# Performance work log

Hardware: AMD Instinct MI355X
Metric: run time of the kernel (lower is better)

## Reference

```python
import jax, jax.numpy as jnp
import numpy as np

B, S, D, VOCAB = 64, 2048, 256, 288

def setup_inputs() -> dict:
    key = jax.random.key(0)
    k1, k2, k3 = jax.random.split(key, 3)
    TE = jax.random.randint(k1, (B, S, 2), 0, VOCAB, dtype=jnp.int64)
    W1 = jax.random.normal(k2, (VOCAB + 7, D), dtype=jnp.float32) * 0.05
    b1 = jnp.zeros((D,), dtype=jnp.float32)
    W2 = jax.random.normal(k3, (D, D), dtype=jnp.float32) * 0.05
    b2 = jnp.zeros((D,), dtype=jnp.float32)
    return {"TE": TE, "T": VOCAB, "W1": W1, "b1": b1, "W2": W2, "b2": b2}

def reference(TE, T, W1, b1, W2, b2):
    # one_hot(day,7)||one_hot(time,T) @ W1  ==  gather rows of W1 and add
    day = TE[..., 0].astype(jnp.int32) % 7          # [B, S]
    tod = TE[..., 1].astype(jnp.int32) % T          # [B, S]
    h = W1[day] + W1[7 + tod] + b1                  # [B, S, D]  (Linear 1)
    h = jax.nn.relu(h)
    out = jnp.einsum('bsd,de->bse', h, W2) + b2     # [B, S, D]  (Linear 2)
    return out[:, :, None, :]                       # [B, S, 1, D]
```

## Files before the change

kernel.cpp:

```cpp
#include <hip/hip_runtime.h>
#include <hip/hip_bf16.h>


typedef __bf16 bf16x4 __attribute__((ext_vector_type(4)));
typedef __bf16 bf16x8 __attribute__((ext_vector_type(8)));
typedef float  f32x4  __attribute__((ext_vector_type(4)));

#define M_TOTAL   131072
#define BM        128
#define HPAD      258


__global__ __launch_bounds__(64) void prep_all(const float* __restrict__ W1,
                                               const float* __restrict__ b1,
                                               const float* __restrict__ W2,
                                               __bf16* __restrict__ W2S,
                                               __bf16* __restrict__ Htab,
                                               const int* __restrict__ TE32,
                                               int* __restrict__ flag, int T) {
    const int b = blockIdx.x, lane = threadIdx.x;
    const int nTab = 7 * T;
    if (b < nTab) {
        const float* __restrict__ wa = W1 + (b / T) * 256;
        const float* __restrict__ wb = W1 + (7 + b % T) * 256;
        f32x4 a = *(const f32x4*)(wa + lane * 4);
        f32x4 c = *(const f32x4*)(wb + lane * 4);
        f32x4 d = *(const f32x4*)(b1 + lane * 4);
        bf16x4 h;
#pragma unroll
        for (int j = 0; j < 4; ++j) h[j] = (__bf16)fmaxf(a[j] + c[j] + d[j], 0.0f);
        *(bf16x4*)(Htab + b * 256 + lane * 4) = h;
    } else {
        const int wb = b - nTab;
#pragma unroll
        for (int q = 0; q < 2; ++q) {
            int c = (wb * 64 + lane) * 2 + q;
            int l = c & 63, ksnt = c >> 6;
            int ks = ksnt & 7, nt = ksnt >> 3;
            int n  = nt * 16 + (l & 15);
            int k0 = ks * 32 + (l >> 4) * 8;
            bf16x8 w;
#pragma unroll
            for (int j = 0; j < 8; ++j) w[j] = (__bf16)W2[(k0 + j) * 256 + n];
            *(bf16x8*)(W2S + c * 8) = w;
        }
        if (wb == 0) {
            int v = 0;
            for (int i = lane; i < 2048; i += 64) v |= TE32[2 * i + 1];
            unsigned long long nz = __ballot(v != 0);
            if (lane == 0) *flag = (nz == 0ull) ? 1 : 0;
        }
    }
}

__global__ __launch_bounds__(256, 4) void temb_gemm(
        const int*   __restrict__ TE32,
        const __bf16* __restrict__ Htab,
        const __bf16* __restrict__ W2S,
        const float* __restrict__ b2,
        const int*   __restrict__ flag,
        float* __restrict__ out, int T)
{
    __shared__ __bf16 hbuf[4][16 * HPAD];
    const int is64 = *flag;
    const int wave = threadIdx.x >> 6;
    const int lane = threadIdx.x & 63;
    const int m    = lane & 15;
    const int quad = lane >> 4;
    const int half = lane >> 5;
    const int c32  = lane & 31;
    const int rowBase = blockIdx.x * BM + wave * 32;
    __bf16* __restrict__ myH = &hbuf[wave][0];

    int code = 0;
    if (lane < 32) {
        int day, tod;
        if (is64) { int4 te = *(const int4*)(TE32 + 4 * (rowBase + lane)); day = te.x; tod = te.z; }
        else      { int2 te = *(const int2*)(TE32 + 2 * (rowBase + lane)); day = te.x; tod = te.y; }
        code = (day % 7) * T + tod % T;
    }

    bf16x8 afrag[2][8];
#pragma unroll
    for (int t = 0; t < 2; ++t) {
#pragma unroll
        for (int g = 0; g < 8; ++g) {
            const int ridx = __shfl(code, t * 16 + 2 * g + half);
            bf16x8 hv = *(const bf16x8*)(Htab + ridx * 256 + c32 * 8);
            *(bf16x8*)(myH + (2 * g + half) * HPAD + c32 * 8) = hv;
        }
#pragma unroll
        for (int ks = 0; ks < 8; ++ks)
            afrag[t][ks] = *(const bf16x8*)(myH + m * HPAD + ks * 32 + quad * 8);
    }

    float b2r[16];
#pragma unroll
    for (int nt = 0; nt < 16; ++nt) b2r[nt] = b2[nt * 16 + m];

    const __bf16* __restrict__ wp = W2S + lane * 8;
#pragma unroll 4
    for (int nt = 0; nt < 16; ++nt) {
        f32x4 acc0 = {0.f, 0.f, 0.f, 0.f};
        f32x4 acc1 = {0.f, 0.f, 0.f, 0.f};
#pragma unroll
        for (int ks = 0; ks < 8; ++ks) {
            bf16x8 bfrag = *(const bf16x8*)(wp + (nt * 8 + ks) * 512);
            acc0 = __builtin_amdgcn_mfma_f32_16x16x32_bf16(afrag[0][ks], bfrag, acc0, 0, 0, 0);
            acc1 = __builtin_amdgcn_mfma_f32_16x16x32_bf16(afrag[1][ks], bfrag, acc1, 0, 0, 0);
        }
        const int ncol = nt * 16 + m;
        const float bias = b2r[nt];
#pragma unroll
        for (int r = 0; r < 4; ++r) {
            const int row0 = rowBase + quad * 4 + r;
            out[row0 * 256 + ncol]        = acc0[r] + bias;
            out[(row0 + 16) * 256 + ncol] = acc1[r] + bias;
        }
    }
}

extern "C" void kernel_launch(void* const* d_in, const int* in_sizes, int n_in,
                              void* d_out, int out_size, void* d_ws, size_t ws_size,
                              hipStream_t stream) {
    const int*   TE = (const int*)  d_in[0];
    const float* W1 = (const float*)d_in[2];
    const float* b1 = (const float*)d_in[3];
    const float* W2 = (const float*)d_in[4];
    const float* b2 = (const float*)d_in[5];
    const int T = in_sizes[2] / 256 - 7;

    __bf16* W2S  = (__bf16*)d_ws;
    __bf16* Htab = (__bf16*)((char*)d_ws + 131072);
    int*    flag = (int*)((char*)d_ws + 131072 + (size_t)7 * T * 256 * 2);
    float*  out  = (float*)d_out;

    prep_all<<<7 * T + 64, 64, 0, stream>>>(W1, b1, W2, W2S, Htab, TE, flag, T);
    temb_gemm<<<M_TOTAL / BM, 256, 0, stream>>>(TE, Htab, W2S, b2, flag, out, T);
}
```

Before: 178.2 us.

## Stage W2 through shared memory and swap MFMA operands for vectorized stores

The GEMM kernel no longer gathers H rows through LDS; each lane loads its H fragments directly from the precomputed table. W2 tiles are now cooperatively staged into shared memory in four double-buffered-by-register chunks, so each block reads them once rather than once per wave. MFMA operands are swapped so each lane owns contiguous output columns, which allows 16-byte vector stores with vector bias loads. This adds block-wide barriers and lowers the occupancy hint from 4 to 3.

```diff
diff --git a/kernel.cpp b/kernel.cpp
--- a/kernel.cpp
+++ b/kernel.cpp
@@ -8,7 +8,6 @@
 
 #define M_TOTAL   131072
 #define BM        128
-#define HPAD      258
 
 
 __global__ __launch_bounds__(64) void prep_all(const float* __restrict__ W1,
@@ -53,7 +52,7 @@
     }
 }
 
-__global__ __launch_bounds__(256, 4) void temb_gemm(
+__global__ __launch_bounds__(256, 3) void temb_gemm(
         const int*   __restrict__ TE32,
         const __bf16* __restrict__ Htab,
         const __bf16* __restrict__ W2S,
@@ -61,62 +60,68 @@
         const int*   __restrict__ flag,
         float* __restrict__ out, int T)
 {
-    __shared__ __bf16 hbuf[4][16 * HPAD];
+    __shared__ __bf16 Bs[4 * 8 * 512];
+
     const int is64 = *flag;
-    const int wave = threadIdx.x >> 6;
-    const int lane = threadIdx.x & 63;
+    const int tid  = threadIdx.x;
+    const int wave = tid >> 6;
+    const int lane = tid & 63;
     const int m    = lane & 15;
     const int quad = lane >> 4;
-    const int half = lane >> 5;
-    const int c32  = lane & 31;
     const int rowBase = blockIdx.x * BM + wave * 32;
-    __bf16* __restrict__ myH = &hbuf[wave][0];
 
-    int code = 0;
-    if (lane < 32) {
-        int day, tod;
-        if (is64) { int4 te = *(const int4*)(TE32 + 4 * (rowBase + lane)); day = te.x; tod = te.z; }
-        else      { int2 te = *(const int2*)(TE32 + 2 * (rowBase + lane)); day = te.x; tod = te.y; }
-        code = (day % 7) * T + tod % T;
-    }
-
-    bf16x8 afrag[2][8];
+    int code[2];
 #pragma unroll
     for (int t = 0; t < 2; ++t) {
+        const int row = rowBase + t * 16 + m;
+        int day, tod;
+        if (is64) { int4 te = *(const int4*)(TE32 + 4 * row); day = te.x; tod = te.z; }
+        else      { int2 te = *(const int2*)(TE32 + 2 * row); day = te.x; tod = te.y; }
+        code[t] = (day % 7) * T + (tod % T);
+    }
+    bf16x8 hfrag[2][8];
 #pragma unroll
-        for (int g = 0; g < 8; ++g) {
-            const int ridx = __shfl(code, t * 16 + 2 * g + half);
-            bf16x8 hv = *(const bf16x8*)(Htab + ridx * 256 + c32 * 8);
-            *(bf16x8*)(myH + (2 * g + half) * HPAD + c32 * 8) = hv;
+    for (int t = 0; t < 2; ++t)
+#pragma unroll
+        for (int ks = 0; ks < 8; ++ks)
+            hfrag[t][ks] = *(const bf16x8*)(Htab + code[t] * 256 + ks * 32 + quad * 8);
+
+    const bf16x8* __restrict__ gsrc = (const bf16x8*)W2S + tid;
+    bf16x8* __restrict__ ldst = (bf16x8*)Bs + tid;
+    const bf16x8* __restrict__ lsrc = (const bf16x8*)Bs;
+
+    bf16x8 stage[8];
+#pragma unroll
+    for (int q = 0; q < 8; ++q) stage[q] = gsrc[q * 256];
+
+    for (int g = 0; g < 4; ++g) {
+#pragma unroll
+        for (int q = 0; q < 8; ++q) ldst[q * 256] = stage[q];
+        __syncthreads();
+        if (g < 3) {
+#pragma unroll
+            for (int q = 0; q < 8; ++q) stage[q] = gsrc[(g + 1) * 2048 + q * 256];
         }
 #pragma unroll
-        for (int ks = 0; ks < 8; ++ks)
-            afrag[t][ks] = *(const bf16x8*)(myH + m * HPAD + ks * 32 + quad * 8);
-    }
-
-    float b2r[16];
+        for (int ntl = 0; ntl < 4; ++ntl) {
+            const int nt = g * 4 + ntl;
+            f32x4 acc0 = {0.f, 0.f, 0.f, 0.f};
+            f32x4 acc1 = {0.f, 0.f, 0.f, 0.f};
 #pragma unroll
-    for (int nt = 0; nt < 16; ++nt) b2r[nt] = b2[nt * 16 + m];
-
-    const __bf16* __restrict__ wp = W2S + lane * 8;
-#pragma unroll 4
-    for (int nt = 0; nt < 16; ++nt) {
-        f32x4 acc0 = {0.f, 0.f, 0.f, 0.f};
-        f32x4 acc1 = {0.f, 0.f, 0.f, 0.f};
+            for (int ks = 0; ks < 8; ++ks) {
+                bf16x8 wfrag = lsrc[(ntl * 8 + ks) * 64 + lane];
+                acc0 = __builtin_amdgcn_mfma_f32_16x16x32_bf16(wfrag, hfrag[0][ks], acc0, 0, 0, 0);
+                acc1 = __builtin_amdgcn_mfma_f32_16x16x32_bf16(wfrag, hfrag[1][ks], acc1, 0, 0, 0);
+            }
+            const f32x4 bias = *(const f32x4*)(b2 + nt * 16 + quad * 4);
+            f32x4 v0, v1;
 #pragma unroll
-        for (int ks = 0; ks < 8; ++ks) {
-            bf16x8 bfrag = *(const bf16x8*)(wp + (nt * 8 + ks) * 512);
-            acc0 = __builtin_amdgcn_mfma_f32_16x16x32_bf16(afrag[0][ks], bfrag, acc0, 0, 0, 0);
-            acc1 = __builtin_amdgcn_mfma_f32_16x16x32_bf16(afrag[1][ks], bfrag, acc1, 0, 0, 0);
+            for (int r = 0; r < 4; ++r) { v0[r] = acc0[r] + bias[r]; v1[r] = acc1[r] + bias[r]; }
+            float* p0 = out + (rowBase + m) * 256 + nt * 16 + quad * 4;
+            *(f32x4*)p0 = v0;
+            *(f32x4*)(p0 + 16 * 256) = v1;
         }
-        const int ncol = nt * 16 + m;
-        const float bias = b2r[nt];
-#pragma unroll
-        for (int r = 0; r < 4; ++r) {
-            const int row0 = rowBase + quad * 4 + r;
-            out[row0 * 256 + ncol]        = acc0[r] + bias;
-            out[(row0 + 16) * 256 + ncol] = acc1[r] + bias;
-        }
+        __syncthreads();
     }
 }
 
@@ -132,7 +137,7 @@
 
     __bf16* W2S  = (__bf16*)d_ws;
     __bf16* Htab = (__bf16*)((char*)d_ws + 131072);
-    int*    flag = (int*)((char*)d_ws + 131072 + (size_t)7 * T * 256 * 2);
+    int*    flag = (int*)((char*)d_ws + 131072 + (size_t)7 * T * 512);
     float*  out  = (float*)d_out;
 
     prep_all<<<7 * T + 64, 64, 0, stream>>>(W1, b1, W2, W2S, Htab, TE, flag, T);
```

New measurement: 165.2 us. 7.3% less time.
